# Performance work log

Measured on AMD Instinct MI355X. Metric: run time of the kernel, lower is better.

The kernel has to match this reference:

```python
import jax, jax.numpy as jnp
import numpy as np

H, I, E, TOPK = 2048, 4096, 8, 2
B, S = 2, 2048

def setup_inputs() -> dict:
    key = jax.random.key(0)
    ks = jax.random.split(key, 6)
    x = jax.random.normal(ks[0], (B, S, H), dtype=jnp.float32)
    expert_indices = jax.random.randint(ks[1], (B, S, TOPK), 0, E, dtype=jnp.int64)
    expert_weights = jax.random.uniform(ks[2], (B, S, TOPK), dtype=jnp.float32)
    gate_proj = jax.random.normal(ks[3], (E, I, H), dtype=jnp.float32) * 0.02
    up_proj = jax.random.normal(ks[4], (E, I, H), dtype=jnp.float32) * 0.02
    down_proj = jax.random.normal(ks[5], (E, H, I), dtype=jnp.float32) * 0.02
    return {"x": x, "expert_indices": expert_indices, "expert_weights": expert_weights,
            "gate_proj": gate_proj, "up_proj": up_proj, "down_proj": down_proj}

def reference(x, expert_indices, expert_weights, gate_proj, up_proj, down_proj):
    b, s, h = x.shape
    T = b * s
    xf = x.reshape(T, h)                                   # [T, H]
    idx = expert_indices.reshape(T, -1)                    # [T, K]
    w = expert_weights.reshape(T, -1)                      # [T, K]
    n_exp = gate_proj.shape[0]
    # Per-token combined weight for each expert (sums duplicate slots, matching
    # the original weighted scatter-add over (token, slot) pairs).
    onehot = jax.nn.one_hot(idx, n_exp, dtype=xf.dtype)    # [T, K, E]
    we = jnp.einsum('tk,tke->et', w, onehot)               # [E, T]

    def step(acc, inp):
        g_w, u_w, d_w, w_e = inp                           # [I,H], [I,H], [H,I], [T]
        g = xf @ g_w.T                                     # [T, I]
        u = xf @ u_w.T                                     # [T, I]
        inter = g * jax.nn.sigmoid(g) * u                  # fused SiLU(g) * u
        acc = acc + w_e[:, None] * (inter @ d_w.T)         # weighted combine
        return acc, None

    out0 = jnp.zeros((T, h), dtype=x.dtype)
    out, _ = jax.lax.scan(step, out0, (gate_proj, up_proj, down_proj, we))
    return out.reshape(b, s, h)
```

## Files before the change

### kernel.cpp

```cpp
#include <hip/hip_runtime.h>
#include <hip/hip_bf16.h>
#include <stdint.h>

#define H_DIM 2048
#define I_DIM 4096
#define NEXP  8
#define NTOK  4096
#define NPAIR 8192
#define PAD_ROWS (NPAIR + 128)

#define WS_COUNTS   0ull
#define WS_OFFSETS  256ull
#define WS_TOKID    1024ull
#define WS_PAIRW    (64ull * 1024)
#define WS_XG       (1ull * 1024 * 1024)
#define WS_INTER    (40ull * 1024 * 1024)
#define WS_NEEDED   (WS_INTER + (unsigned long long)PAD_ROWS * I_DIM * 2)

typedef __attribute__((ext_vector_type(8))) short bf16x8;
typedef __attribute__((ext_vector_type(4))) float f32x4;

#if defined(__has_builtin)
#if __has_builtin(__builtin_amdgcn_cvt_pk_bf16_f32)
#define HAVE_CVT_PK 1
#endif
#endif

__device__ __forceinline__ uint32_t bf16_bits_rne(float x) {
  uint32_t u = __float_as_uint(x);
  return (u + 0x7FFFu + ((u >> 16) & 1u)) >> 16;
}

__device__ __forceinline__ uint32_t pk_bf16(float a, float b) {
#ifdef HAVE_CVT_PK
  auto r = __builtin_amdgcn_cvt_pk_bf16_f32(a, b);
  return __builtin_bit_cast(uint32_t, r);
#else
  return bf16_bits_rne(a) | (bf16_bits_rne(b) << 16);
#endif
}

__device__ __forceinline__ uint16_t bf16_one(float x) {
  return (uint16_t)(pk_bf16(x, x) & 0xFFFFu);
}

__device__ __forceinline__ void async_load16(const void* g, void* l) {
  __builtin_amdgcn_global_load_lds(
      (const __attribute__((address_space(1))) void*)g,
      (__attribute__((address_space(3))) void*)l, 16, 0, 0);
}

__global__ void route_kernel(const int* __restrict__ idx, const float* __restrict__ wts,
                             int* __restrict__ ws_counts, int* __restrict__ ws_offsets,
                             int* __restrict__ tokid, float* __restrict__ pairw) {
  __shared__ int s_cnt[NEXP], s_off[NEXP], s_cur[NEXP];
  int tid = threadIdx.x;
  if (tid < NEXP) s_cnt[tid] = 0;
  __syncthreads();
  for (int p = tid; p < NPAIR; p += 256) atomicAdd(&s_cnt[idx[p]], 1);
  __syncthreads();
  if (tid == 0) {
    int acc = 0;
    for (int e = 0; e < NEXP; e++) { s_off[e] = acc; s_cur[e] = acc; acc += s_cnt[e]; }
  }
  __syncthreads();
  for (int p = tid; p < NPAIR; p += 256) {
    int e = idx[p];
    int slot = atomicAdd(&s_cur[e], 1);
    tokid[slot] = p >> 1;
    pairw[slot] = wts[p];
  }
  if (tid < NEXP) { ws_counts[tid] = s_cnt[tid]; ws_offsets[tid] = s_off[tid]; }
}

__global__ void gather_cast_kernel(const float* __restrict__ x, const int* __restrict__ tokid,
                                   uint16_t* __restrict__ xg) {
  int p = blockIdx.x;
  int t = tokid[p];
  int c = threadIdx.x * 8;
  const float4* src = (const float4*)(x + (size_t)t * H_DIM + c);
  float4 v0 = src[0], v1 = src[1];
  uint4 o;
  o.x = pk_bf16(v0.x, v0.y); o.y = pk_bf16(v0.z, v0.w);
  o.z = pk_bf16(v1.x, v1.y); o.w = pk_bf16(v1.z, v1.w);
  *(uint4*)(xg + (size_t)p * H_DIM + c) = o;
}

__global__ __launch_bounds__(256, 2)
void gemm1_kernel(const uint16_t* __restrict__ xg,
                  const float* __restrict__ gate, const float* __restrict__ up,
                  const int* __restrict__ ws_counts, const int* __restrict__ ws_offsets,
                  uint16_t* __restrict__ inter) {
  int e = blockIdx.z;
  int cnt = ws_counts[e];
  int rowTile = blockIdx.y;
  if (rowTile * 128 >= cnt) return;
  int off = ws_offsets[e];
  int colBase = blockIdx.x * 128;
  size_t rowBase = (size_t)off + (size_t)rowTile * 128;

  __shared__ uint16_t lA[128 * 64];
  __shared__ uint16_t lBg[128 * 64];
  __shared__ uint16_t lBu[128 * 64];

  int tid = threadIdx.x;
  int lane = tid & 63, wid = tid >> 6;
  int wm = (wid & 1) * 64, wn = (wid >> 1) * 64;
  int lcol = lane & 15, quad = lane >> 4;

  const float* gbase = gate + (size_t)e * I_DIM * H_DIM + (size_t)colBase * H_DIM;
  const float* ubase = up   + (size_t)e * I_DIM * H_DIM + (size_t)colBase * H_DIM;

  f32x4 accg[4][4], accu[4][4];
  f32x4 zero = {0.f, 0.f, 0.f, 0.f};
#pragma unroll
  for (int mi = 0; mi < 4; mi++)
#pragma unroll
    for (int ni = 0; ni < 4; ni++) { accg[mi][ni] = zero; accu[mi][ni] = zero; }

  for (int k0 = 0; k0 < H_DIM; k0 += 64) {
    __syncthreads();
#pragma unroll
    for (int rd = 0; rd < 4; rd++) {
      int chunkBase = rd * 256 + wid * 64;
      int chunk = chunkBase + lane;
      int row = chunk >> 3, kc = (chunk & 7) * 8;
      async_load16(xg + (rowBase + row) * H_DIM + k0 + kc, lA + chunkBase * 8);
    }
#pragma unroll
    for (int it = 0; it < 4; it++) {
      int c = it * 256 + tid;
      int row = c >> 3, kc = (c & 7) * 8;
      size_t soff = (size_t)row * H_DIM + k0 + kc;
      const float4* sg = (const float4*)(gbase + soff);
      float4 g0 = sg[0], g1 = sg[1];
      const float4* su = (const float4*)(ubase + soff);
      float4 u0 = su[0], u1 = su[1];
      uint4 og = { pk_bf16(g0.x, g0.y), pk_bf16(g0.z, g0.w), pk_bf16(g1.x, g1.y), pk_bf16(g1.z, g1.w) };
      uint4 ou = { pk_bf16(u0.x, u0.y), pk_bf16(u0.z, u0.w), pk_bf16(u1.x, u1.y), pk_bf16(u1.z, u1.w) };
      *(uint4*)(lBg + c * 8) = og;
      *(uint4*)(lBu + c * 8) = ou;
    }
    __syncthreads();
#pragma unroll
    for (int ks = 0; ks < 64; ks += 32) {
      int krow = ks + quad * 8;
      bf16x8 af[4], bg[4], bu[4];
#pragma unroll
      for (int mi = 0; mi < 4; mi++)
        af[mi] = *(const bf16x8*)(lA + (wm + mi * 16 + lcol) * 64 + krow);
#pragma unroll
      for (int ni = 0; ni < 4; ni++) {
        bg[ni] = *(const bf16x8*)(lBg + (wn + ni * 16 + lcol) * 64 + krow);
        bu[ni] = *(const bf16x8*)(lBu + (wn + ni * 16 + lcol) * 64 + krow);
      }
#pragma unroll
      for (int mi = 0; mi < 4; mi++)
#pragma unroll
        for (int ni = 0; ni < 4; ni++) {
          accg[mi][ni] = __builtin_amdgcn_mfma_f32_16x16x32_bf16(af[mi], bg[ni], accg[mi][ni], 0, 0, 0);
          accu[mi][ni] = __builtin_amdgcn_mfma_f32_16x16x32_bf16(af[mi], bu[ni], accu[mi][ni], 0, 0, 0);
        }
    }
  }
  int col0 = colBase + wn;
#pragma unroll
  for (int mi = 0; mi < 4; mi++) {
#pragma unroll
    for (int r = 0; r < 4; r++) {
      int localRow = rowTile * 128 + wm + mi * 16 + quad * 4 + r;
      if (localRow < cnt) {
        size_t prow = (size_t)off + localRow;
#pragma unroll
        for (int ni = 0; ni < 4; ni++) {
          float g = accg[mi][ni][r], u = accu[mi][ni][r];
          float v = (g / (1.f + __expf(-g))) * u;
          inter[prow * I_DIM + col0 + ni * 16 + lcol] = bf16_one(v);
        }
      }
    }
  }
}

__global__ __launch_bounds__(256, 2)
void gemm2_kernel(const uint16_t* __restrict__ inter, const float* __restrict__ down,
                  const int* __restrict__ ws_counts, const int* __restrict__ ws_offsets,
                  const int* __restrict__ tokid, const float* __restrict__ pairw,
                  float* __restrict__ out) {
  int e = blockIdx.z;
  int cnt = ws_counts[e];
  int rowTile = blockIdx.y;
  if (rowTile * 128 >= cnt) return;
  int off = ws_offsets[e];
  int colBase = blockIdx.x * 128;
  size_t rowBase = (size_t)off + (size_t)rowTile * 128;

  __shared__ uint16_t lA[128 * 64];
  __shared__ uint16_t lB[128 * 64];

  int tid = threadIdx.x;
  int lane = tid & 63, wid = tid >> 6;
  int wm = (wid & 1) * 64, wn = (wid >> 1) * 64;
  int lcol = lane & 15, quad = lane >> 4;

  const float* dbase = down + (size_t)e * H_DIM * I_DIM + (size_t)colBase * I_DIM;

  f32x4 acc[4][4];
  f32x4 zero = {0.f, 0.f, 0.f, 0.f};
#pragma unroll
  for (int mi = 0; mi < 4; mi++)
#pragma unroll
    for (int ni = 0; ni < 4; ni++) acc[mi][ni] = zero;

  for (int k0 = 0; k0 < I_DIM; k0 += 64) {
    __syncthreads();
#pragma unroll
    for (int rd = 0; rd < 4; rd++) {
      int chunkBase = rd * 256 + wid * 64;
      int chunk = chunkBase + lane;
      int row = chunk >> 3, kc = (chunk & 7) * 8;
      async_load16(inter + (rowBase + row) * I_DIM + k0 + kc, lA + chunkBase * 8);
    }
#pragma unroll
    for (int it = 0; it < 4; it++) {
      int c = it * 256 + tid;
      int row = c >> 3, kc = (c & 7) * 8;
      const float4* sd = (const float4*)(dbase + (size_t)row * I_DIM + k0 + kc);
      float4 d0 = sd[0], d1 = sd[1];
      uint4 od = { pk_bf16(d0.x, d0.y), pk_bf16(d0.z, d0.w), pk_bf16(d1.x, d1.y), pk_bf16(d1.z, d1.w) };
      *(uint4*)(lB + c * 8) = od;
    }
    __syncthreads();
#pragma unroll
    for (int ks = 0; ks < 64; ks += 32) {
      int krow = ks + quad * 8;
      bf16x8 af[4], bf[4];
#pragma unroll
      for (int mi = 0; mi < 4; mi++)
        af[mi] = *(const bf16x8*)(lA + (wm + mi * 16 + lcol) * 64 + krow);
#pragma unroll
      for (int ni = 0; ni < 4; ni++)
        bf[ni] = *(const bf16x8*)(lB + (wn + ni * 16 + lcol) * 64 + krow);
#pragma unroll
      for (int mi = 0; mi < 4; mi++)
#pragma unroll
        for (int ni = 0; ni < 4; ni++)
          acc[mi][ni] = __builtin_amdgcn_mfma_f32_16x16x32_bf16(af[mi], bf[ni], acc[mi][ni], 0, 0, 0);
    }
  }
  int col0 = colBase + wn;
#pragma unroll
  for (int mi = 0; mi < 4; mi++) {
#pragma unroll
    for (int r = 0; r < 4; r++) {
      int localRow = rowTile * 128 + wm + mi * 16 + quad * 4 + r;
      if (localRow < cnt) {
        size_t prow = (size_t)off + localRow;
        int t = tokid[prow];
        float w = pairw[prow];
        float* orow = out + (size_t)t * H_DIM + col0;
#pragma unroll
        for (int ni = 0; ni < 4; ni++)
          atomicAdd(orow + ni * 16 + lcol, acc[mi][ni][r] * w);
      }
    }
  }
}

extern "C" void kernel_launch(void* const* d_in, const int* in_sizes, int n_in,
                              void* d_out, int out_size, void* d_ws, size_t ws_size,
                              hipStream_t stream) {
  const float* x    = (const float*)d_in[0];
  const int*   eidx = (const int*)d_in[1];
  const float* ew   = (const float*)d_in[2];
  const float* gate = (const float*)d_in[3];
  const float* up   = (const float*)d_in[4];
  const float* down = (const float*)d_in[5];
  float* out = (float*)d_out;
  char* ws = (char*)d_ws;

  if (ws_size < WS_NEEDED) {
    hipMemsetAsync(d_out, 0, (size_t)NTOK * H_DIM * sizeof(float), stream);
    return;
  }

  int*      counts  = (int*)(ws + WS_COUNTS);
  int*      offsets = (int*)(ws + WS_OFFSETS);
  int*      tokid   = (int*)(ws + WS_TOKID);
  float*    pairw   = (float*)(ws + WS_PAIRW);
  uint16_t* xg      = (uint16_t*)(ws + WS_XG);
  uint16_t* inter   = (uint16_t*)(ws + WS_INTER);

  hipMemsetAsync(d_out, 0, (size_t)NTOK * H_DIM * sizeof(float), stream);
  route_kernel<<<1, 256, 0, stream>>>(eidx, ew, counts, offsets, tokid, pairw);
  gather_cast_kernel<<<NPAIR, 256, 0, stream>>>(x, tokid, xg);
  gemm1_kernel<<<dim3(I_DIM / 128, NPAIR / 128, NEXP), 256, 0, stream>>>(
      xg, gate, up, counts, offsets, inter);
  gemm2_kernel<<<dim3(H_DIM / 128, NPAIR / 128, NEXP), 256, 0, stream>>>(
      inter, down, counts, offsets, tokid, pairw, out);
}
```

Baseline: 1.415 ms.

## Pre-cast weights to bf16, triple-buffer async GEMMs, replace atomics with combine pass

```diff
diff --git a/kernel.cpp b/kernel.cpp
--- a/kernel.cpp
+++ b/kernel.cpp
@@ -7,15 +7,21 @@
 #define NEXP  8
 #define NTOK  4096
 #define NPAIR 8192
-#define PAD_ROWS (NPAIR + 128)
-
+#define PAD_ROWS (NPAIR + 256)
+
+#define MiB (1024ull * 1024ull)
 #define WS_COUNTS   0ull
 #define WS_OFFSETS  256ull
 #define WS_TOKID    1024ull
-#define WS_PAIRW    (64ull * 1024)
-#define WS_XG       (1ull * 1024 * 1024)
-#define WS_INTER    (40ull * 1024 * 1024)
-#define WS_NEEDED   (WS_INTER + (unsigned long long)PAD_ROWS * I_DIM * 2)
+#define WS_SLOT     (64ull * 1024)
+#define WS_PAIRW    (128ull * 1024)
+#define WS_XG       (1ull * MiB)
+#define WS_INTER    (36ull * MiB)
+#define WS_Y        (104ull * MiB)
+#define WS_GW       (176ull * MiB)
+#define WS_UW       (304ull * MiB)
+#define WS_DW       (432ull * MiB)
+#define WS_FULL     (560ull * MiB)
 
 typedef __attribute__((ext_vector_type(8))) short bf16x8;
 typedef __attribute__((ext_vector_type(4))) float f32x4;
@@ -30,7 +36,6 @@
   uint32_t u = __float_as_uint(x);
   return (u + 0x7FFFu + ((u >> 16) & 1u)) >> 16;
 }
-
 __device__ __forceinline__ uint32_t pk_bf16(float a, float b) {
 #ifdef HAVE_CVT_PK
   auto r = __builtin_amdgcn_cvt_pk_bf16_f32(a, b);
@@ -39,7 +44,6 @@
   return bf16_bits_rne(a) | (bf16_bits_rne(b) << 16);
 #endif
 }
-
 __device__ __forceinline__ uint16_t bf16_one(float x) {
   return (uint16_t)(pk_bf16(x, x) & 0xFFFFu);
 }
@@ -50,9 +54,14 @@
       (__attribute__((address_space(3))) void*)l, 16, 0, 0);
 }
 
+#define WAIT_VM6()  do { asm volatile("s_waitcnt vmcnt(6)" ::: "memory"); __builtin_amdgcn_sched_barrier(0); } while (0)
+#define WAIT_VM0()  do { asm volatile("s_waitcnt vmcnt(0)" ::: "memory"); __builtin_amdgcn_sched_barrier(0); } while (0)
+#define BARRIER()   do { __builtin_amdgcn_s_barrier(); asm volatile("" ::: "memory"); } while (0)
+
 __global__ void route_kernel(const int* __restrict__ idx, const float* __restrict__ wts,
                              int* __restrict__ ws_counts, int* __restrict__ ws_offsets,
-                             int* __restrict__ tokid, float* __restrict__ pairw) {
+                             int* __restrict__ tokid, int* __restrict__ slotOf,
+                             float* __restrict__ pairw) {
   __shared__ int s_cnt[NEXP], s_off[NEXP], s_cur[NEXP];
   int tid = threadIdx.x;
   if (tid < NEXP) s_cnt[tid] = 0;
@@ -68,6 +77,7 @@
     int e = idx[p];
     int slot = atomicAdd(&s_cur[e], 1);
     tokid[slot] = p >> 1;
+    slotOf[p] = slot;
     pairw[slot] = wts[p];
   }
   if (tid < NEXP) { ws_counts[tid] = s_cnt[tid]; ws_offsets[tid] = s_off[tid]; }
@@ -86,93 +96,121 @@
   *(uint4*)(xg + (size_t)p * H_DIM + c) = o;
 }
 
-__global__ __launch_bounds__(256, 2)
-void gemm1_kernel(const uint16_t* __restrict__ xg,
-                  const float* __restrict__ gate, const float* __restrict__ up,
-                  const int* __restrict__ ws_counts, const int* __restrict__ ws_offsets,
-                  uint16_t* __restrict__ inter) {
+__global__ void cast3_kernel(const float* __restrict__ g, const float* __restrict__ u,
+                             const float* __restrict__ d,
+                             uint16_t* __restrict__ gw, uint16_t* __restrict__ uw,
+                             uint16_t* __restrict__ dw) {
+  const float* src = blockIdx.y == 0 ? g : (blockIdx.y == 1 ? u : d);
+  uint16_t*    dst = blockIdx.y == 0 ? gw : (blockIdx.y == 1 ? uw : dw);
+  const long long n8 = (long long)NEXP * I_DIM * H_DIM / 8;
+  long long stride = (long long)gridDim.x * blockDim.x;
+  for (long long i = (long long)blockIdx.x * blockDim.x + threadIdx.x; i < n8; i += stride) {
+    const float4* s = (const float4*)(src + i * 8);
+    float4 a = s[0], b = s[1];
+    uint4 o = { pk_bf16(a.x, a.y), pk_bf16(a.z, a.w), pk_bf16(b.x, b.y), pk_bf16(b.z, b.w) };
+    *(uint4*)(dst + i * 8) = o;
+  }
+}
+
+#define T1_A    (256 * 64)
+#define T1_B    (64 * 64)
+#define T1_ELE  (T1_A + 2 * T1_B)
+
+__global__ __launch_bounds__(512, 1)
+void gemm1_v2(const uint16_t* __restrict__ xg,
+              const uint16_t* __restrict__ gw, const uint16_t* __restrict__ uw,
+              const int* __restrict__ ws_counts, const int* __restrict__ ws_offsets,
+              uint16_t* __restrict__ inter) {
   int e = blockIdx.z;
   int cnt = ws_counts[e];
   int rowTile = blockIdx.y;
-  if (rowTile * 128 >= cnt) return;
+  if (rowTile * 256 >= cnt) return;
   int off = ws_offsets[e];
-  int colBase = blockIdx.x * 128;
-  size_t rowBase = (size_t)off + (size_t)rowTile * 128;
-
-  __shared__ uint16_t lA[128 * 64];
-  __shared__ uint16_t lBg[128 * 64];
-  __shared__ uint16_t lBu[128 * 64];
-
-  int tid = threadIdx.x;
-  int lane = tid & 63, wid = tid >> 6;
-  int wm = (wid & 1) * 64, wn = (wid >> 1) * 64;
+  int colBase = blockIdx.x * 64;
+  size_t rowBase = (size_t)off + (size_t)rowTile * 256;
+
+  __shared__ uint16_t lds[3 * T1_ELE];
+
+  int tid = threadIdx.x, lane = tid & 63, w = tid >> 6;
+  int r8 = lane >> 3;
+  int gsw = ((lane & 7) ^ r8) << 3;
+
+  const uint16_t* srcA[4];
+#pragma unroll
+  for (int c = 0; c < 4; c++)
+    srcA[c] = xg + (rowBase + (size_t)(w * 32 + c * 8 + r8)) * H_DIM + gsw;
+  const uint16_t* srcG = gw + ((size_t)e * I_DIM + colBase + w * 8 + r8) * H_DIM + gsw;
+  const uint16_t* srcU = uw + ((size_t)e * I_DIM + colBase + w * 8 + r8) * H_DIM + gsw;
+
+  const int dA = w * 2048;
+  const int dG = T1_A + w * 512;
+  const int dU = T1_A + T1_B + w * 512;
+
+  f32x4 accg[4][2], accu[4][2];
+  f32x4 zero = {0.f, 0.f, 0.f, 0.f};
+#pragma unroll
+  for (int mi = 0; mi < 4; mi++)
+#pragma unroll
+    for (int ni = 0; ni < 2; ni++) { accg[mi][ni] = zero; accu[mi][ni] = zero; }
+
+  auto STG = [&](int kt, int b) {
+    uint16_t* lb = lds + b * T1_ELE;
+    int ko = kt * 64;
+#pragma unroll
+    for (int c = 0; c < 4; c++) async_load16(srcA[c] + ko, lb + dA + c * 512);
+    async_load16(srcG + ko, lb + dG);
+    async_load16(srcU + ko, lb + dU);
+  };
+
+  STG(0, 0); STG(1, 1);
+  WAIT_VM6();
+  BARRIER();
+
+  int wr = w >> 1, wc = w & 1;
+  int wm = wr * 64, wn = wc * 32;
   int lcol = lane & 15, quad = lane >> 4;
-
-  const float* gbase = gate + (size_t)e * I_DIM * H_DIM + (size_t)colBase * H_DIM;
-  const float* ubase = up   + (size_t)e * I_DIM * H_DIM + (size_t)colBase * H_DIM;
-
-  f32x4 accg[4][4], accu[4][4];
-  f32x4 zero = {0.f, 0.f, 0.f, 0.f};
-#pragma unroll
-  for (int mi = 0; mi < 4; mi++)
-#pragma unroll
-    for (int ni = 0; ni < 4; ni++) { accg[mi][ni] = zero; accu[mi][ni] = zero; }
-
-  for (int k0 = 0; k0 < H_DIM; k0 += 64) {
-    __syncthreads();
-#pragma unroll
-    for (int rd = 0; rd < 4; rd++) {
-      int chunkBase = rd * 256 + wid * 64;
-      int chunk = chunkBase + lane;
-      int row = chunk >> 3, kc = (chunk & 7) * 8;
-      async_load16(xg + (rowBase + row) * H_DIM + k0 + kc, lA + chunkBase * 8);
+  int sx = (lcol & 7) << 3;
+
+  const int NT = H_DIM / 64;
+  for (int t = 0; t < NT; ++t) {
+    if (t + 2 < NT) STG(t + 2, (t + 2) % 3);
+    const uint16_t* lb = lds + (t % 3) * T1_ELE;
+#pragma unroll
+    for (int ks = 0; ks < 2; ks++) {
+      int krs = (ks * 32 + quad * 8) ^ sx;
+      bf16x8 af[4], bg_[2], bu_[2];
+#pragma unroll
+      for (int mi = 0; mi < 4; mi++)
+        af[mi] = *(const bf16x8*)(lb + (wm + mi * 16 + lcol) * 64 + krs);
+#pragma unroll
+      for (int ni = 0; ni < 2; ni++) {
+        bg_[ni] = *(const bf16x8*)(lb + T1_A + (wn + ni * 16 + lcol) * 64 + krs);
+        bu_[ni] = *(const bf16x8*)(lb + T1_A + T1_B + (wn + ni * 16 + lcol) * 64 + krs);
+      }
+      __builtin_amdgcn_s_setprio(1);
+#pragma unroll
+      for (int mi = 0; mi < 4; mi++)
+#pragma unroll
+        for (int ni = 0; ni < 2; ni++) {
+          accg[mi][ni] = __builtin_amdgcn_mfma_f32_16x16x32_bf16(af[mi], bg_[ni], accg[mi][ni], 0, 0, 0);
+          accu[mi][ni] = __builtin_amdgcn_mfma_f32_16x16x32_bf16(af[mi], bu_[ni], accu[mi][ni], 0, 0, 0);
+        }
+      __builtin_amdgcn_s_setprio(0);
     }
-#pragma unroll
-    for (int it = 0; it < 4; it++) {
-      int c = it * 256 + tid;
-      int row = c >> 3, kc = (c & 7) * 8;
-      size_t soff = (size_t)row * H_DIM + k0 + kc;
-      const float4* sg = (const float4*)(gbase + soff);
-      float4 g0 = sg[0], g1 = sg[1];
-      const float4* su = (const float4*)(ubase + soff);
-      float4 u0 = su[0], u1 = su[1];
-      uint4 og = { pk_bf16(g0.x, g0.y), pk_bf16(g0.z, g0.w), pk_bf16(g1.x, g1.y), pk_bf16(g1.z, g1.w) };
-      uint4 ou = { pk_bf16(u0.x, u0.y), pk_bf16(u0.z, u0.w), pk_bf16(u1.x, u1.y), pk_bf16(u1.z, u1.w) };
-      *(uint4*)(lBg + c * 8) = og;
-      *(uint4*)(lBu + c * 8) = ou;
-    }
-    __syncthreads();
-#pragma unroll
-    for (int ks = 0; ks < 64; ks += 32) {
-      int krow = ks + quad * 8;
-      bf16x8 af[4], bg[4], bu[4];
-#pragma unroll
-      for (int mi = 0; mi < 4; mi++)
-        af[mi] = *(const bf16x8*)(lA + (wm + mi * 16 + lcol) * 64 + krow);
-#pragma unroll
-      for (int ni = 0; ni < 4; ni++) {
-        bg[ni] = *(const bf16x8*)(lBg + (wn + ni * 16 + lcol) * 64 + krow);
-        bu[ni] = *(const bf16x8*)(lBu + (wn + ni * 16 + lcol) * 64 + krow);
-      }
-#pragma unroll
-      for (int mi = 0; mi < 4; mi++)
-#pragma unroll
-        for (int ni = 0; ni < 4; ni++) {
-          accg[mi][ni] = __builtin_amdgcn_mfma_f32_16x16x32_bf16(af[mi], bg[ni], accg[mi][ni], 0, 0, 0);
-          accu[mi][ni] = __builtin_amdgcn_mfma_f32_16x16x32_bf16(af[mi], bu[ni], accu[mi][ni], 0, 0, 0);
-        }
-    }
-  }
+    if (t + 2 < NT) { WAIT_VM6(); } else { WAIT_VM0(); }
+    BARRIER();
+  }
+
   int col0 = colBase + wn;
 #pragma unroll
   for (int mi = 0; mi < 4; mi++) {
 #pragma unroll
     for (int r = 0; r < 4; r++) {
-      int localRow = rowTile * 128 + wm + mi * 16 + quad * 4 + r;
+      int localRow = rowTile * 256 + wm + mi * 16 + quad * 4 + r;
       if (localRow < cnt) {
         size_t prow = (size_t)off + localRow;
 #pragma unroll
-        for (int ni = 0; ni < 4; ni++) {
+        for (int ni = 0; ni < 2; ni++) {
           float g = accg[mi][ni][r], u = accu[mi][ni][r];
           float v = (g / (1.f + __expf(-g))) * u;
           inter[prow * I_DIM + col0 + ni * 16 + lcol] = bf16_one(v);
@@ -182,28 +220,39 @@
   }
 }
 
-__global__ __launch_bounds__(256, 2)
-void gemm2_kernel(const uint16_t* __restrict__ inter, const float* __restrict__ down,
-                  const int* __restrict__ ws_counts, const int* __restrict__ ws_offsets,
-                  const int* __restrict__ tokid, const float* __restrict__ pairw,
-                  float* __restrict__ out) {
+#define T2_A    (256 * 64)
+#define T2_B    (128 * 64)
+#define T2_ELE  (T2_A + T2_B)
+
+__global__ __launch_bounds__(512, 1)
+void gemm2_v2(const uint16_t* __restrict__ inter, const uint16_t* __restrict__ dw,
+              const int* __restrict__ ws_counts, const int* __restrict__ ws_offsets,
+              const float* __restrict__ pairw, float* __restrict__ y) {
   int e = blockIdx.z;
   int cnt = ws_counts[e];
   int rowTile = blockIdx.y;
-  if (rowTile * 128 >= cnt) return;
+  if (rowTile * 256 >= cnt) return;
   int off = ws_offsets[e];
   int colBase = blockIdx.x * 128;
-  size_t rowBase = (size_t)off + (size_t)rowTile * 128;
-
-  __shared__ uint16_t lA[128 * 64];
-  __shared__ uint16_t lB[128 * 64];
-
-  int tid = threadIdx.x;
-  int lane = tid & 63, wid = tid >> 6;
-  int wm = (wid & 1) * 64, wn = (wid >> 1) * 64;
-  int lcol = lane & 15, quad = lane >> 4;
-
-  const float* dbase = down + (size_t)e * H_DIM * I_DIM + (size_t)colBase * I_DIM;
+  size_t rowBase = (size_t)off + (size_t)rowTile * 256;
+
+  __shared__ uint16_t lds[3 * T2_ELE];
+
+  int tid = threadIdx.x, lane = tid & 63, w = tid >> 6;
+  int r8 = lane >> 3;
+  int gsw = ((lane & 7) ^ r8) << 3;
+
+  const uint16_t* srcA[4];
+#pragma unroll
+  for (int c = 0; c < 4; c++)
+    srcA[c] = inter + (rowBase + (size_t)(w * 32 + c * 8 + r8)) * I_DIM + gsw;
+  const uint16_t* srcB[2];
+#pragma unroll
+  for (int c = 0; c < 2; c++)
+    srcB[c] = dw + ((size_t)e * H_DIM + colBase + w * 16 + c * 8 + r8) * I_DIM + gsw;
+
+  const int dA = w * 2048;
+  const int dB = T2_A + w * 1024;
 
   f32x4 acc[4][4];
   f32x4 zero = {0.f, 0.f, 0.f, 0.f};
@@ -212,59 +261,80 @@
 #pragma unroll
     for (int ni = 0; ni < 4; ni++) acc[mi][ni] = zero;
 
-  for (int k0 = 0; k0 < I_DIM; k0 += 64) {
-    __syncthreads();
-#pragma unroll
-    for (int rd = 0; rd < 4; rd++) {
-      int chunkBase = rd * 256 + wid * 64;
-      int chunk = chunkBase + lane;
-      int row = chunk >> 3, kc = (chunk & 7) * 8;
-      async_load16(inter + (rowBase + row) * I_DIM + k0 + kc, lA + chunkBase * 8);
+  auto STG = [&](int kt, int b) {
+    uint16_t* lb = lds + b * T2_ELE;
+    int ko = kt * 64;
+#pragma unroll
+    for (int c = 0; c < 4; c++) async_load16(srcA[c] + ko, lb + dA + c * 512);
+#pragma unroll
+    for (int c = 0; c < 2; c++) async_load16(srcB[c] + ko, lb + dB + c * 512);
+  };
+
+  STG(0, 0); STG(1, 1);
+  WAIT_VM6();
+  BARRIER();
+
+  int wr = w >> 1, wc = w & 1;
+  int wm = wr * 64, wn = wc * 64;
+  int lcol = lane & 15, quad = lane >> 4;
+  int sx = (lcol & 7) << 3;
+
+  const int NT = I_DIM / 64;
+  for (int t = 0; t < NT; ++t) {
+    if (t + 2 < NT) STG(t + 2, (t + 2) % 3);
+    const uint16_t* lb = lds + (t % 3) * T2_ELE;
+#pragma unroll
+    for (int ks = 0; ks < 2; ks++) {
+      int krs = (ks * 32 + quad * 8) ^ sx;
+      bf16x8 af[4], bf_[4];
+#pragma unroll
+      for (int mi = 0; mi < 4; mi++)
+        af[mi] = *(const bf16x8*)(lb + (wm + mi * 16 + lcol) * 64 + krs);
+#pragma unroll
+      for (int ni = 0; ni < 4; ni++)
+        bf_[ni] = *(const bf16x8*)(lb + T2_A + (wn + ni * 16 + lcol) * 64 + krs);
+      __builtin_amdgcn_s_setprio(1);
+#pragma unroll
+      for (int mi = 0; mi < 4; mi++)
+#pragma unroll
+        for (int ni = 0; ni < 4; ni++)
+          acc[mi][ni] = __builtin_amdgcn_mfma_f32_16x16x32_bf16(af[mi], bf_[ni], acc[mi][ni], 0, 0, 0);
+      __builtin_amdgcn_s_setprio(0);
     }
-#pragma unroll
-    for (int it = 0; it < 4; it++) {
-      int c = it * 256 + tid;
-      int row = c >> 3, kc = (c & 7) * 8;
-      const float4* sd = (const float4*)(dbase + (size_t)row * I_DIM + k0 + kc);
-      float4 d0 = sd[0], d1 = sd[1];
-      uint4 od = { pk_bf16(d0.x, d0.y), pk_bf16(d0.z, d0.w), pk_bf16(d1.x, d1.y), pk_bf16(d1.z, d1.w) };
-      *(uint4*)(lB + c * 8) = od;
-    }
-    __syncthreads();
-#pragma unroll
-    for (int ks = 0; ks < 64; ks += 32) {
-      int krow = ks + quad * 8;
-      bf16x8 af[4], bf[4];
-#pragma unroll
-      for (int mi = 0; mi < 4; mi++)
-        af[mi] = *(const bf16x8*)(lA + (wm + mi * 16 + lcol) * 64 + krow);
-#pragma unroll
-      for (int ni = 0; ni < 4; ni++)
-        bf[ni] = *(const bf16x8*)(lB + (wn + ni * 16 + lcol) * 64 + krow);
-#pragma unroll
-      for (int mi = 0; mi < 4; mi++)
-#pragma unroll
-        for (int ni = 0; ni < 4; ni++)
-          acc[mi][ni] = __builtin_amdgcn_mfma_f32_16x16x32_bf16(af[mi], bf[ni], acc[mi][ni], 0, 0, 0);
-    }
-  }
+    if (t + 2 < NT) { WAIT_VM6(); } else { WAIT_VM0(); }
+    BARRIER();
+  }
+
   int col0 = colBase + wn;
 #pragma unroll
   for (int mi = 0; mi < 4; mi++) {
 #pragma unroll
     for (int r = 0; r < 4; r++) {
-      int localRow = rowTile * 128 + wm + mi * 16 + quad * 4 + r;
+      int localRow = rowTile * 256 + wm + mi * 16 + quad * 4 + r;
       if (localRow < cnt) {
         size_t prow = (size_t)off + localRow;
-        int t = tokid[prow];
-        float w = pairw[prow];
-        float* orow = out + (size_t)t * H_DIM + col0;
+        float wgt = pairw[prow];
+        float* yr = y + prow * H_DIM + col0;
 #pragma unroll
         for (int ni = 0; ni < 4; ni++)
-          atomicAdd(orow + ni * 16 + lcol, acc[mi][ni][r] * w);
+          yr[ni * 16 + lcol] = acc[mi][ni][r] * wgt;
       }
     }
   }
+}
+
+__global__ void combine_kernel(const float* __restrict__ y, const int* __restrict__ slotOf,
+                               float* __restrict__ out) {
+  int t = blockIdx.x;
+  int s0 = slotOf[2 * t], s1 = slotOf[2 * t + 1];
+  int c = threadIdx.x * 8;
+  const float4* a = (const float4*)(y + (size_t)s0 * H_DIM + c);
+  const float4* b = (const float4*)(y + (size_t)s1 * H_DIM + c);
+  float4 a0 = a[0], a1 = a[1], b0 = b[0], b1 = b[1];
+  float4 o0 = {a0.x + b0.x, a0.y + b0.y, a0.z + b0.z, a0.w + b0.w};
+  float4 o1 = {a1.x + b1.x, a1.y + b1.y, a1.z + b1.z, a1.w + b1.w};
+  float4* dst = (float4*)(out + (size_t)t * H_DIM + c);
+  dst[0] = o0; dst[1] = o1;
 }
 
 extern "C" void kernel_launch(void* const* d_in, const int* in_sizes, int n_in,
@@ -279,7 +349,7 @@
   float* out = (float*)d_out;
   char* ws = (char*)d_ws;
 
-  if (ws_size < WS_NEEDED) {
+  if (ws_size < WS_FULL) {
     hipMemsetAsync(d_out, 0, (size_t)NTOK * H_DIM * sizeof(float), stream);
     return;
   }
@@ -287,15 +357,22 @@
   int*      counts  = (int*)(ws + WS_COUNTS);
   int*      offsets = (int*)(ws + WS_OFFSETS);
   int*      tokid   = (int*)(ws + WS_TOKID);
+  int*      slotOf  = (int*)(ws + WS_SLOT);
   float*    pairw   = (float*)(ws + WS_PAIRW);
   uint16_t* xg      = (uint16_t*)(ws + WS_XG);
   uint16_t* inter   = (uint16_t*)(ws + WS_INTER);
-
-  hipMemsetAsync(d_out, 0, (size_t)NTOK * H_DIM * sizeof(float), stream);
-  route_kernel<<<1, 256, 0, stream>>>(eidx, ew, counts, offsets, tokid, pairw);
+  float*    y       = (float*)(ws + WS_Y);
+  uint16_t* gw      = (uint16_t*)(ws + WS_GW);
+  uint16_t* uw      = (uint16_t*)(ws + WS_UW);
+  uint16_t* dwp     = (uint16_t*)(ws + WS_DW);
+
+  route_kernel<<<1, 256, 0, stream>>>(eidx, ew, counts, offsets, tokid, slotOf, pairw);
   gather_cast_kernel<<<NPAIR, 256, 0, stream>>>(x, tokid, xg);
-  gemm1_kernel<<<dim3(I_DIM / 128, NPAIR / 128, NEXP), 256, 0, stream>>>(
-      xg, gate, up, counts, offsets, inter);
-  gemm2_kernel<<<dim3(H_DIM / 128, NPAIR / 128, NEXP), 256, 0, stream>>>(
-      inter, down, counts, offsets, tokid, pairw, out);
-}
+  cast3_kernel<<<dim3(2048, 3), 256, 0, stream>>>(gate, up, down, gw, uw, dwp);
+
+  gemm1_v2<<<dim3(I_DIM / 64, NPAIR / 256, NEXP), 512, 0, stream>>>(
+      xg, gw, uw, counts, offsets, inter);
+  gemm2_v2<<<dim3(H_DIM / 128, NPAIR / 256, NEXP), 512, 0, stream>>>(
+      inter, dwp, counts, offsets, pairw, y);
+  combine_kernel<<<NTOK, 256, 0, stream>>>(y, slotOf, out);
+}
```

New measurement: 1.333 ms. 5.8% less time.
